# Performance work log

Hardware: AMD Instinct MI355X
Metric: run time of the kernel (lower is better)

Reference implementation:

```python
import jax, jax.numpy as jnp
import numpy as np

N = 100000
E = 1600000
NEG_SLOPE = 0.2


def _param(key, shape, scale=0.05):
    return jax.random.normal(key, shape, dtype=jnp.float32) * scale


def setup_inputs() -> dict:
    key = jax.random.key(0)
    ks = jax.random.split(key, 16)
    x = jax.random.normal(ks[0], (N, 128), dtype=jnp.float32)
    edge_index = jax.random.randint(ks[1], (2, E), 0, N, dtype=jnp.int64)
    # layer 1: 128 -> (H=2, C=64), concat
    W1 = _param(ks[2], (128, 2 * 64)); a_src1 = _param(ks[3], (2, 64)); a_dst1 = _param(ks[4], (2, 64)); b1 = jnp.zeros((128,), jnp.float32)
    # layer 2: 128 -> (H=2, C=64), concat
    W2 = _param(ks[5], (128, 2 * 64)); a_src2 = _param(ks[6], (2, 64)); a_dst2 = _param(ks[7], (2, 64)); b2 = jnp.zeros((128,), jnp.float32)
    # layer 3: 128 -> (H=1, C=64), mean (concat=False)
    W3 = _param(ks[8], (128, 1 * 64)); a_src3 = _param(ks[9], (1, 64)); a_dst3 = _param(ks[10], (1, 64)); b3 = jnp.zeros((64,), jnp.float32)
    return {"x": x, "edge_index": edge_index,
            "W1": W1, "a_src1": a_src1, "a_dst1": a_dst1, "b1": b1,
            "W2": W2, "a_src2": a_src2, "a_dst2": a_dst2, "b2": b2,
            "W3": W3, "a_src3": a_src3, "a_dst3": a_dst3, "b3": b3}


def gat_layer(x, src, dst, W, a_src, a_dst, b, concat):
    H, C = a_src.shape
    n = x.shape[0]
    h = (x @ W).reshape(n, H, C)                      # [N,H,C]
    # per-node attention logits (avoid [E,H,C] gather for the score step)
    al_s = jnp.sum(h * a_src[None], axis=-1)          # [N,H]
    al_d = jnp.sum(h * a_dst[None], axis=-1)          # [N,H]
    e = al_s[src] + al_d[dst]                         # [E',H]
    e = jnp.where(e > 0, e, NEG_SLOPE * e)            # LeakyReLU(0.2)
    # scatter-softmax over incoming edges per destination node
    m = jax.ops.segment_max(e, dst, num_segments=n)   # [N,H]
    ex = jnp.exp(e - m[dst])
    z = jax.ops.segment_sum(ex, dst, num_segments=n)  # [N,H]
    alpha = ex / z[dst]                               # [E',H]
    msg = h[src] * alpha[:, :, None]                  # [E',H,C]
    out = jax.ops.segment_sum(msg, dst, num_segments=n)  # [N,H,C]
    out = out.reshape(n, H * C) if concat else out.mean(axis=1)
    return out + b


def reference(x, edge_index, W1, a_src1, a_dst1, b1, W2, a_src2, a_dst2, b2, W3, a_src3, a_dst3, b3):
    n = x.shape[0]
    loop = jnp.arange(n, dtype=edge_index.dtype)
    src = jnp.concatenate([edge_index[0], loop])      # add self-loops (PyG default)
    dst = jnp.concatenate([edge_index[1], loop])
    h = gat_layer(x, src, dst, W1, a_src1, a_dst1, b1, True)
    h = jax.nn.relu(h)
    h = gat_layer(h, src, dst, W2, a_src2, a_dst2, b2, True)
    h = jax.nn.relu(h)
    return gat_layer(h, src, dst, W3, a_src3, a_dst3, b3, False)
```

## Files before the change

### kernel.cpp

```cpp
#include <hip/hip_runtime.h>

#define NEG_SLOPE 0.2f
#define BUK_SHIFT 9
#define BUK_SIZE 512
#define BUK_CAP 16384

typedef unsigned short u16;
typedef __attribute__((ext_vector_type(4))) float f4v;
typedef _Float16 h8 __attribute__((ext_vector_type(8)));

__device__ __forceinline__ u16 f2h_bits(_Float16 h) {
    union { _Float16 f; u16 u; } c;
    c.f = h;
    return c.u;
}


__launch_bounds__(256)
__global__ void k_binscatter(const int* __restrict__ ei, int* g_cnt, int* buckets,
                             int E, int nb) {
    __shared__ int lcnt[256], lbase[256], lcur[256];
    int t = threadIdx.x;
    if (t < nb) {
        lcnt[t] = 0;
        lcur[t] = 0;
    }
    __syncthreads();
    int tile0 = blockIdx.x * 4096;
    int pk[16], bk[16];
#pragma unroll
    for (int k = 0; k < 16; k++) {
        int idx = tile0 + k * 256 + t;
        bk[k] = -1;
        if (idx < E) {
            int s = ei[idx];
            int d = ei[E + idx];
            bk[k] = d >> BUK_SHIFT;
            pk[k] = (s << BUK_SHIFT) | (d & (BUK_SIZE - 1));
            atomicAdd(&lcnt[bk[k]], 1);
        }
    }
    __syncthreads();
    if (t < nb && lcnt[t] > 0) lbase[t] = atomicAdd(&g_cnt[t], lcnt[t]);
    __syncthreads();
#pragma unroll
    for (int k = 0; k < 16; k++) {
        if (bk[k] >= 0) {
            int p = lbase[bk[k]] + atomicAdd(&lcur[bk[k]], 1);
            if (p < BUK_CAP) buckets[(bk[k] << 14) + p] = pk[k];
        }
    }
}

__launch_bounds__(512)
__global__ void k_csr(const int* __restrict__ g_cnt, const int* __restrict__ buckets,
                      int* csr_ptr, int* csr_src, int n, int nb) {
    __shared__ int lcnt[512], lsc[512], lcur[512], bsc[512];
    int b = blockIdx.x;
    int t = threadIdx.x;
    int nodes = min(BUK_SIZE, n - b * BUK_SIZE);
    int cnt = min(g_cnt[b], BUK_CAP);
    const int* bp = &buckets[b << 14];

    int bv = 0;
    if (t < nb) bv = min(g_cnt[t], BUK_CAP) + min(BUK_SIZE, n - t * BUK_SIZE);
    bsc[t] = bv;
    __syncthreads();
    for (int off = 1; off < 512; off <<= 1) {
        int x = (t >= off) ? bsc[t - off] : 0;
        __syncthreads();
        bsc[t] += x;
        __syncthreads();
    }
    int boff = bsc[b] - (cnt + nodes);
    int total = bsc[nb - 1];
    __syncthreads();

    lcnt[t] = 0;
    __syncthreads();
    for (int i = t; i < cnt; i += 512) atomicAdd(&lcnt[bp[i] & (BUK_SIZE - 1)], 1);
    __syncthreads();
    int myc = (t < nodes) ? (lcnt[t] + 1) : 0;
    lsc[t] = myc;
    __syncthreads();
    for (int off = 1; off < 512; off <<= 1) {
        int x = (t >= off) ? lsc[t - off] : 0;
        __syncthreads();
        lsc[t] += x;
        __syncthreads();
    }
    int excl = lsc[t] - myc;
    lcur[t] = excl;
    if (t < nodes) csr_ptr[b * BUK_SIZE + t] = boff + excl;
    if (b == nb - 1 && t == 0) csr_ptr[n] = total;
    __syncthreads();
    for (int i = t; i < cnt; i += 512) {
        int v = bp[i];
        int ld = v & (BUK_SIZE - 1);
        int p = atomicAdd(&lcur[ld], 1);
        csr_src[boff + p] = v >> BUK_SHIFT;
    }
    if (t < nodes) {
        int p = atomicAdd(&lcur[t], 1);
        csr_src[boff + p] = b * BUK_SIZE + t;
    }
}


__global__ void k_wsplit_all(const float* __restrict__ W1, const float* __restrict__ W2,
                             const float* __restrict__ W3, u16* __restrict__ T1h,
                             u16* __restrict__ T1l, u16* __restrict__ T2h,
                             u16* __restrict__ T2l, u16* __restrict__ T3h,
                             u16* __restrict__ T3l, int* __restrict__ g_cnt) {
    int t = blockIdx.x * 256 + threadIdx.x;
    if (t < 256) g_cnt[t] = 0;
    const float* W;
    u16 *Th, *Tl;
    int M, idx;
    if (t < 16384) {
        W = W1; Th = T1h; Tl = T1l; M = 128; idx = t;
    } else if (t < 32768) {
        W = W2; Th = T2h; Tl = T2l; M = 128; idx = t - 16384;
    } else if (t < 40960) {
        W = W3; Th = T3h; Tl = T3l; M = 64; idx = t - 32768;
    } else {
        return;
    }
    int c = idx >> 7, k = idx & 127;
    float v = W[(size_t)k * M + c];
    _Float16 h = (_Float16)v;
    _Float16 l = (_Float16)(v - (float)h);
    int ct = c >> 4, ch = k >> 5, q = (k >> 3) & 3, j = k & 7;
    size_t addr = ((size_t)ct * 4 + ch) * 512 + ((c & 15) + 16 * q) * 8 + j;
    Th[addr] = f2h_bits(h);
    Tl[addr] = f2h_bits(l);
}


__global__ void k_wa(const float* __restrict__ W1, const float* __restrict__ as1,
                     const float* __restrict__ ad1, const float* __restrict__ W2,
                     const float* __restrict__ as2, const float* __restrict__ ad2,
                     const float* __restrict__ W3, const float* __restrict__ as3,
                     const float* __restrict__ ad3, u16* __restrict__ T1h,
                     u16* __restrict__ T1l, u16* __restrict__ T2h, u16* __restrict__ T2l,
                     u16* __restrict__ T3h, u16* __restrict__ T3l) {
    int t = blockIdx.x * 256 + threadIdx.x;
    if (t >= 6144) return;
    int layer = t >> 11;
    int rem = t & 2047;
    int k = rem >> 4;
    int c = rem & 15;
    const float *W, *as, *ad;
    u16 *Th, *Tl;
    int M, CT, nc;
    if (layer == 0) {
        W = W1; as = as1; ad = ad1; Th = T1h; Tl = T1l; M = 128; CT = 8; nc = 4;
    } else if (layer == 1) {
        W = W2; as = as2; ad = ad2; Th = T2h; Tl = T2l; M = 128; CT = 8; nc = 4;
    } else {
        W = W3; as = as3; ad = ad3; Th = T3h; Tl = T3l; M = 64; CT = 4; nc = 2;
    }
    float val = 0.f;
    if (c < nc) {
        int side, hh;
        if (nc == 4) { side = c >> 1; hh = c & 1; }
        else { side = c; hh = 0; }
        const float* a = side ? ad : as;
        for (int j = 0; j < 64; j++)
            val += W[(size_t)k * M + hh * 64 + j] * a[hh * 64 + j];
    }
    _Float16 h = (_Float16)val;
    _Float16 l = (_Float16)(val - (float)h);
    int ch = k >> 5, q = (k >> 3) & 3, j = k & 7;
    size_t addr = ((size_t)CT * 4 + ch) * 512 + ((size_t)(c + 16 * q)) * 8 + j;
    Th[addr] = f2h_bits(h);
    Tl[addr] = f2h_bits(l);
}


__device__ __forceinline__ void load_split_f32(const float* __restrict__ X, int row,
                                               int koff, int N, h8& hi, h8& lo) {
    float v[8];
    if (row < N) {
        float4 a = *(const float4*)&X[(size_t)row * 128 + koff];
        float4 b = *(const float4*)&X[(size_t)row * 128 + koff + 4];
        v[0] = a.x; v[1] = a.y; v[2] = a.z; v[3] = a.w;
        v[4] = b.x; v[5] = b.y; v[6] = b.z; v[7] = b.w;
    } else {
#pragma unroll
        for (int i = 0; i < 8; i++) v[i] = 0.f;
    }
    union { h8 s; _Float16 u[8]; } H, L;
#pragma unroll
    for (int i = 0; i < 8; i++) {
        H.u[i] = (_Float16)v[i];
        L.u[i] = (_Float16)(v[i] - (float)H.u[i]);
    }
    hi = H.s;
    lo = L.s;
}

template <int M, bool FP32X>
__launch_bounds__(256)
__global__ void k_gemm_mfma(const float* __restrict__ Xf, const u16* __restrict__ XH,
                            const u16* __restrict__ WTh, const u16* __restrict__ WTl,
                            _Float16* __restrict__ Hout, float* __restrict__ als,
                            float* __restrict__ ald, int nrows) {
    const int CT = M / 16;
    const int CTX = CT + 1;
    const int H = (M == 128) ? 2 : 1;
    int tid = threadIdx.x;
    int wv = tid >> 6, lane = tid & 63;
    int q = lane >> 4, nl = lane & 15;
    int R0 = blockIdx.x * 128 + wv * 32;
    int rt0 = R0 >> 4;

    f4v acc[2][CTX];
    f4v z4 = {0.f, 0.f, 0.f, 0.f};
#pragma unroll
    for (int rt = 0; rt < 2; rt++)
#pragma unroll
        for (int ct = 0; ct < CTX; ct++) acc[rt][ct] = z4;

#pragma unroll
    for (int ch = 0; ch < 4; ch++) {
        h8 ah0, al0, ah1, al1;
        if (FP32X) {
            int koff = ch * 32 + q * 8;
            load_split_f32(Xf, R0 + nl, koff, nrows, ah0, al0);
            load_split_f32(Xf, R0 + 16 + nl, koff, nrows, ah1, al1);
        } else {
            size_t a0 = ((size_t)rt0 * 4 + ch) * 512 + lane * 8;
            size_t a1 = ((size_t)(rt0 + 1) * 4 + ch) * 512 + lane * 8;
            ah0 = *(const h8*)&XH[a0];
            ah1 = *(const h8*)&XH[a1];
        }
#pragma unroll
        for (int ct = 0; ct < CTX; ct++) {
            size_t bb = ((size_t)ct * 4 + ch) * 512 + lane * 8;
            h8 bh = *(const h8*)&WTh[bb];
            h8 bl = *(const h8*)&WTl[bb];
            acc[0][ct] = __builtin_amdgcn_mfma_f32_16x16x32_f16(ah0, bh, acc[0][ct], 0, 0, 0);
            acc[0][ct] = __builtin_amdgcn_mfma_f32_16x16x32_f16(ah0, bl, acc[0][ct], 0, 0, 0);
            acc[1][ct] = __builtin_amdgcn_mfma_f32_16x16x32_f16(ah1, bh, acc[1][ct], 0, 0, 0);
            acc[1][ct] = __builtin_amdgcn_mfma_f32_16x16x32_f16(ah1, bl, acc[1][ct], 0, 0, 0);
            if (FP32X) {
                acc[0][ct] = __builtin_amdgcn_mfma_f32_16x16x32_f16(al0, bh, acc[0][ct], 0, 0, 0);
                acc[1][ct] = __builtin_amdgcn_mfma_f32_16x16x32_f16(al1, bh, acc[1][ct], 0, 0, 0);
            }
        }
    }

#pragma unroll
    for (int rt = 0; rt < 2; rt++)
#pragma unroll
        for (int ct = 0; ct < CT; ct++)
#pragma unroll
            for (int r = 0; r < 4; r++) {
                int row = R0 + rt * 16 + q * 4 + r;
                if (row < nrows) Hout[(size_t)row * M + ct * 16 + nl] = (_Float16)acc[rt][ct][r];
            }

    if (nl < 2 * H) {
#pragma unroll
        for (int rt = 0; rt < 2; rt++)
#pragma unroll
            for (int r = 0; r < 4; r++) {
                int row = R0 + rt * 16 + q * 4 + r;
                if (row < nrows) {
                    float v = acc[rt][CT][r];
                    if (H == 2) {
                        float* dstp = (nl < 2) ? als : ald;
                        dstp[(size_t)row * 2 + (nl & 1)] = v;
                    } else {
                        float* dstp = (nl == 0) ? als : ald;
                        dstp[row] = v;
                    }
                }
            }
    }
}


__launch_bounds__(256)
__global__ void k_agg128(const int* __restrict__ ptr, const int* __restrict__ srcv,
                         const _Float16* __restrict__ Hh, const float* __restrict__ als,
                         const float* __restrict__ ald, const float* __restrict__ bias,
                         u16* __restrict__ OutX, int n) {
    int wvg = (blockIdx.x * blockDim.x + threadIdx.x) >> 6;
    int lane = threadIdx.x & 63;
    int nn = lane >> 4;
    int gl = lane & 15;
    int wid = wvg * 4 + nn;
    bool valid = wid < n;
    int widc = valid ? wid : (n - 1);
    int start = ptr[widc];
    int deg = valid ? (ptr[widc + 1] - start) : 0;
    int md = deg;
    md = max(md, __shfl_xor(md, 16));
    md = max(md, __shfl_xor(md, 32));
    float2 adv = *(const float2*)&ald[(size_t)widc * 2];
    int hsel = gl >> 3;
    int coff = gl * 8;
    float z0 = 0.f, z1 = 0.f;
    float acc[8];
#pragma unroll
    for (int c = 0; c < 8; c++) acc[c] = 0.f;

    for (int base = 0; base < md; base += 16) {
        int i = base + gl;
        int s_l = 0;
        float ex0 = 0.f, ex1 = 0.f;
        if (i < deg) {
            s_l = srcv[start + i];
            float2 av = *(const float2*)&als[(size_t)s_l * 2];
            float e0 = av.x + adv.x;
            e0 = e0 > 0.f ? e0 : NEG_SLOPE * e0;
            ex0 = __expf(e0);
            float e1 = av.y + adv.y;
            e1 = e1 > 0.f ? e1 : NEG_SLOPE * e1;
            ex1 = __expf(e1);
        }
        z0 += ex0;
        z1 += ex1;
        int cnt = min(16, md - base);
        for (int jp = 0; jp < cnt; jp += 4) {
            int nk = min(4, cnt - jp);
            h8 hv[4];
            float w[4];
#pragma unroll
            for (int k = 0; k < 4; k++) {
                if (k < nk) {
                    int j = nn * 16 + jp + k;
                    int s = __shfl(s_l, j);
                    float w0 = __shfl(ex0, j);
                    float w1 = __shfl(ex1, j);
                    w[k] = hsel ? w1 : w0;
                    hv[k] = *(const h8*)&Hh[(size_t)s * 128 + coff];
                }
            }
#pragma unroll
            for (int k = 0; k < 4; k++) {
                if (k < nk) {
#pragma unroll
                    for (int c = 0; c < 8; c++)
                        acc[c] = fmaf(w[k], (float)hv[k][c], acc[c]);
                }
            }
        }
    }

#pragma unroll
    for (int m = 1; m <= 8; m <<= 1) {
        z0 += __shfl_xor(z0, m);
        z1 += __shfl_xor(z1, m);
    }
    if (valid) {
        float zinv = hsel ? (1.f / z1) : (1.f / z0);
        float4 b0 = *(const float4*)&bias[coff];
        float4 b1 = *(const float4*)&bias[coff + 4];
        float bb[8] = {b0.x, b0.y, b0.z, b0.w, b1.x, b1.y, b1.z, b1.w};
        union { _Float16 f[8]; h8 v; } O;
#pragma unroll
        for (int c = 0; c < 8; c++) {
            float o = fmaxf(fmaf(acc[c], zinv, bb[c]), 0.f);
            O.f[c] = (_Float16)o;
        }
        int ch = coff >> 5, qq = (coff >> 3) & 3;
        size_t tb = ((size_t)(wid >> 4) * 4 + ch) * 512 + ((size_t)((wid & 15) + 16 * qq)) * 8;
        *(h8*)&OutX[tb] = O.v;
    }
}


__launch_bounds__(256)
__global__ void k_agg64(const int* __restrict__ ptr, const int* __restrict__ srcv,
                        const _Float16* __restrict__ Hh, const float* __restrict__ als,
                        const float* __restrict__ ald, const float* __restrict__ bias,
                        float* __restrict__ Out, int n) {
    int wvg = (blockIdx.x * blockDim.x + threadIdx.x) >> 6;
    int lane = threadIdx.x & 63;
    int nn = lane >> 3;
    int gl = lane & 7;
    int wid = wvg * 8 + nn;
    bool valid = wid < n;
    int widc = valid ? wid : (n - 1);
    int start = ptr[widc];
    int deg = valid ? (ptr[widc + 1] - start) : 0;
    int md = deg;
    md = max(md, __shfl_xor(md, 8));
    md = max(md, __shfl_xor(md, 16));
    md = max(md, __shfl_xor(md, 32));
    float ad0 = ald[widc];
    int coff = gl * 8;
    float z = 0.f;
    float acc[8];
#pragma unroll
    for (int c = 0; c < 8; c++) acc[c] = 0.f;

    for (int base = 0; base < md; base += 8) {
        int i = base + gl;
        int s_l = 0;
        float ex0 = 0.f;
        if (i < deg) {
            s_l = srcv[start + i];
            float e = als[s_l] + ad0;
            e = e > 0.f ? e : NEG_SLOPE * e;
            ex0 = __expf(e);
        }
        z += ex0;
        int cnt = min(8, md - base);
        for (int jp = 0; jp < cnt; jp += 4) {
            int nk = min(4, cnt - jp);
            h8 hv[4];
            float w[4];
#pragma unroll
            for (int k = 0; k < 4; k++) {
                if (k < nk) {
                    int j = nn * 8 + jp + k;
                    int s = __shfl(s_l, j);
                    w[k] = __shfl(ex0, j);
                    hv[k] = *(const h8*)&Hh[(size_t)s * 64 + coff];
                }
            }
#pragma unroll
            for (int k = 0; k < 4; k++) {
                if (k < nk) {
#pragma unroll
                    for (int c = 0; c < 8; c++)
                        acc[c] = fmaf(w[k], (float)hv[k][c], acc[c]);
                }
            }
        }
    }

#pragma unroll
    for (int m = 1; m <= 4; m <<= 1) z += __shfl_xor(z, m);
    if (valid) {
        float zinv = 1.f / z;
        float4 b0 = *(const float4*)&bias[coff];
        float4 b1 = *(const float4*)&bias[coff + 4];
        float4 o1, o2;
        o1.x = fmaf(acc[0], zinv, b0.x);
        o1.y = fmaf(acc[1], zinv, b0.y);
        o1.z = fmaf(acc[2], zinv, b0.z);
        o1.w = fmaf(acc[3], zinv, b0.w);
        o2.x = fmaf(acc[4], zinv, b1.x);
        o2.y = fmaf(acc[5], zinv, b1.y);
        o2.z = fmaf(acc[6], zinv, b1.z);
        o2.w = fmaf(acc[7], zinv, b1.w);
        *(float4*)&Out[(size_t)wid * 64 + coff] = o1;
        *(float4*)&Out[(size_t)wid * 64 + coff + 4] = o2;
    }
}


extern "C" void kernel_launch(void* const* d_in, const int* in_sizes, int n_in,
                              void* d_out, int out_size, void* d_ws, size_t ws_size,
                              hipStream_t stream) {
    const float* x = (const float*)d_in[0];
    const int* ei = (const int*)d_in[1];
    const float* W1 = (const float*)d_in[2];
    const float* as1 = (const float*)d_in[3];
    const float* ad1 = (const float*)d_in[4];
    const float* b1 = (const float*)d_in[5];
    const float* W2 = (const float*)d_in[6];
    const float* as2 = (const float*)d_in[7];
    const float* ad2 = (const float*)d_in[8];
    const float* b2 = (const float*)d_in[9];
    const float* W3 = (const float*)d_in[10];
    const float* as3 = (const float*)d_in[11];
    const float* ad3 = (const float*)d_in[12];
    const float* b3 = (const float*)d_in[13];

    const int N = in_sizes[0] / 128;
    const int E = in_sizes[1] / 2;
    const int NB = (N + BUK_SIZE - 1) / BUK_SIZE;
    const int Npad = (N + 127) & ~127;

    char* p = (char*)d_ws;
    auto alloc = [&](size_t bytes) -> char* {
        char* r = p;
        p += (bytes + 255) & ~(size_t)255;
        return r;
    };
    int* g_cnt = (int*)alloc(256 * 4);
    int* buckets = (int*)alloc((size_t)NB * BUK_CAP * 4);
    int* csr_ptr = (int*)alloc((size_t)(N + 1) * 4);
    int* csr_src = (int*)alloc((size_t)(E + N) * 4);
    float* als = (float*)alloc((size_t)N * 2 * 4);
    float* aldv = (float*)alloc((size_t)N * 2 * 4);
    _Float16* Hbuf = (_Float16*)alloc((size_t)N * 128 * 2);
    u16* XH = (u16*)alloc((size_t)Npad * 128 * 2);
    u16* WT1h = (u16*)alloc(9 * 2048 * 2);
    u16* WT1l = (u16*)alloc(9 * 2048 * 2);
    u16* WT2h = (u16*)alloc(9 * 2048 * 2);
    u16* WT2l = (u16*)alloc(9 * 2048 * 2);
    u16* WT3h = (u16*)alloc(5 * 2048 * 2);
    u16* WT3l = (u16*)alloc(5 * 2048 * 2);

    const int nbG = Npad / 128;
    const int waves128 = (N + 3) / 4;
    const int nbAgg128 = (waves128 + 3) / 4;
    const int waves64 = (N + 7) / 8;
    const int nbAgg64 = (waves64 + 3) / 4;
    const int nbTile = (E + 4095) / 4096;

    k_wsplit_all<<<160, 256, 0, stream>>>(W1, W2, W3, WT1h, WT1l, WT2h, WT2l, WT3h,
                                          WT3l, g_cnt);
    k_wa<<<24, 256, 0, stream>>>(W1, as1, ad1, W2, as2, ad2, W3, as3, ad3,
                                 WT1h, WT1l, WT2h, WT2l, WT3h, WT3l);

    k_binscatter<<<nbTile, 256, 0, stream>>>(ei, g_cnt, buckets, E, NB);
    k_csr<<<NB, 512, 0, stream>>>(g_cnt, buckets, csr_ptr, csr_src, N, NB);

    k_gemm_mfma<128, true><<<nbG, 256, 0, stream>>>(x, nullptr, WT1h, WT1l,
                                                    Hbuf, als, aldv, N);
    k_agg128<<<nbAgg128, 256, 0, stream>>>(csr_ptr, csr_src, Hbuf, als, aldv, b1, XH, N);

    k_gemm_mfma<128, false><<<nbG, 256, 0, stream>>>(nullptr, XH, WT2h, WT2l,
                                                     Hbuf, als, aldv, N);
    k_agg128<<<nbAgg128, 256, 0, stream>>>(csr_ptr, csr_src, Hbuf, als, aldv, b2, XH, N);

    k_gemm_mfma<64, false><<<nbG, 256, 0, stream>>>(nullptr, XH, WT3h, WT3l,
                                                    Hbuf, als, aldv, N);
    k_agg64<<<nbAgg64, 256, 0, stream>>>(csr_ptr, csr_src, Hbuf, als, aldv, b3,
                                         (float*)d_out, N);
}
```

Measured before the change: 418.6 us.

## Merge preprocessing kernels and overlap CSR build with first-layer GEMM

Result: faster. 400.5 us, median of 2 (-4.3%).

```diff
diff --git a/kernel.cpp b/kernel.cpp
--- a/kernel.cpp
+++ b/kernel.cpp
@@ -13,168 +13,6 @@
     union { _Float16 f; u16 u; } c;
     c.f = h;
     return c.u;
-}
-
-
-__launch_bounds__(256)
-__global__ void k_binscatter(const int* __restrict__ ei, int* g_cnt, int* buckets,
-                             int E, int nb) {
-    __shared__ int lcnt[256], lbase[256], lcur[256];
-    int t = threadIdx.x;
-    if (t < nb) {
-        lcnt[t] = 0;
-        lcur[t] = 0;
-    }
-    __syncthreads();
-    int tile0 = blockIdx.x * 4096;
-    int pk[16], bk[16];
-#pragma unroll
-    for (int k = 0; k < 16; k++) {
-        int idx = tile0 + k * 256 + t;
-        bk[k] = -1;
-        if (idx < E) {
-            int s = ei[idx];
-            int d = ei[E + idx];
-            bk[k] = d >> BUK_SHIFT;
-            pk[k] = (s << BUK_SHIFT) | (d & (BUK_SIZE - 1));
-            atomicAdd(&lcnt[bk[k]], 1);
-        }
-    }
-    __syncthreads();
-    if (t < nb && lcnt[t] > 0) lbase[t] = atomicAdd(&g_cnt[t], lcnt[t]);
-    __syncthreads();
-#pragma unroll
-    for (int k = 0; k < 16; k++) {
-        if (bk[k] >= 0) {
-            int p = lbase[bk[k]] + atomicAdd(&lcur[bk[k]], 1);
-            if (p < BUK_CAP) buckets[(bk[k] << 14) + p] = pk[k];
-        }
-    }
-}
-
-__launch_bounds__(512)
-__global__ void k_csr(const int* __restrict__ g_cnt, const int* __restrict__ buckets,
-                      int* csr_ptr, int* csr_src, int n, int nb) {
-    __shared__ int lcnt[512], lsc[512], lcur[512], bsc[512];
-    int b = blockIdx.x;
-    int t = threadIdx.x;
-    int nodes = min(BUK_SIZE, n - b * BUK_SIZE);
-    int cnt = min(g_cnt[b], BUK_CAP);
-    const int* bp = &buckets[b << 14];
-
-    int bv = 0;
-    if (t < nb) bv = min(g_cnt[t], BUK_CAP) + min(BUK_SIZE, n - t * BUK_SIZE);
-    bsc[t] = bv;
-    __syncthreads();
-    for (int off = 1; off < 512; off <<= 1) {
-        int x = (t >= off) ? bsc[t - off] : 0;
-        __syncthreads();
-        bsc[t] += x;
-        __syncthreads();
-    }
-    int boff = bsc[b] - (cnt + nodes);
-    int total = bsc[nb - 1];
-    __syncthreads();
-
-    lcnt[t] = 0;
-    __syncthreads();
-    for (int i = t; i < cnt; i += 512) atomicAdd(&lcnt[bp[i] & (BUK_SIZE - 1)], 1);
-    __syncthreads();
-    int myc = (t < nodes) ? (lcnt[t] + 1) : 0;
-    lsc[t] = myc;
-    __syncthreads();
-    for (int off = 1; off < 512; off <<= 1) {
-        int x = (t >= off) ? lsc[t - off] : 0;
-        __syncthreads();
-        lsc[t] += x;
-        __syncthreads();
-    }
-    int excl = lsc[t] - myc;
-    lcur[t] = excl;
-    if (t < nodes) csr_ptr[b * BUK_SIZE + t] = boff + excl;
-    if (b == nb - 1 && t == 0) csr_ptr[n] = total;
-    __syncthreads();
-    for (int i = t; i < cnt; i += 512) {
-        int v = bp[i];
-        int ld = v & (BUK_SIZE - 1);
-        int p = atomicAdd(&lcur[ld], 1);
-        csr_src[boff + p] = v >> BUK_SHIFT;
-    }
-    if (t < nodes) {
-        int p = atomicAdd(&lcur[t], 1);
-        csr_src[boff + p] = b * BUK_SIZE + t;
-    }
-}
-
-
-__global__ void k_wsplit_all(const float* __restrict__ W1, const float* __restrict__ W2,
-                             const float* __restrict__ W3, u16* __restrict__ T1h,
-                             u16* __restrict__ T1l, u16* __restrict__ T2h,
-                             u16* __restrict__ T2l, u16* __restrict__ T3h,
-                             u16* __restrict__ T3l, int* __restrict__ g_cnt) {
-    int t = blockIdx.x * 256 + threadIdx.x;
-    if (t < 256) g_cnt[t] = 0;
-    const float* W;
-    u16 *Th, *Tl;
-    int M, idx;
-    if (t < 16384) {
-        W = W1; Th = T1h; Tl = T1l; M = 128; idx = t;
-    } else if (t < 32768) {
-        W = W2; Th = T2h; Tl = T2l; M = 128; idx = t - 16384;
-    } else if (t < 40960) {
-        W = W3; Th = T3h; Tl = T3l; M = 64; idx = t - 32768;
-    } else {
-        return;
-    }
-    int c = idx >> 7, k = idx & 127;
-    float v = W[(size_t)k * M + c];
-    _Float16 h = (_Float16)v;
-    _Float16 l = (_Float16)(v - (float)h);
-    int ct = c >> 4, ch = k >> 5, q = (k >> 3) & 3, j = k & 7;
-    size_t addr = ((size_t)ct * 4 + ch) * 512 + ((c & 15) + 16 * q) * 8 + j;
-    Th[addr] = f2h_bits(h);
-    Tl[addr] = f2h_bits(l);
-}
-
-
-__global__ void k_wa(const float* __restrict__ W1, const float* __restrict__ as1,
-                     const float* __restrict__ ad1, const float* __restrict__ W2,
-                     const float* __restrict__ as2, const float* __restrict__ ad2,
-                     const float* __restrict__ W3, const float* __restrict__ as3,
-                     const float* __restrict__ ad3, u16* __restrict__ T1h,
-                     u16* __restrict__ T1l, u16* __restrict__ T2h, u16* __restrict__ T2l,
-                     u16* __restrict__ T3h, u16* __restrict__ T3l) {
-    int t = blockIdx.x * 256 + threadIdx.x;
-    if (t >= 6144) return;
-    int layer = t >> 11;
-    int rem = t & 2047;
-    int k = rem >> 4;
-    int c = rem & 15;
-    const float *W, *as, *ad;
-    u16 *Th, *Tl;
-    int M, CT, nc;
-    if (layer == 0) {
-        W = W1; as = as1; ad = ad1; Th = T1h; Tl = T1l; M = 128; CT = 8; nc = 4;
-    } else if (layer == 1) {
-        W = W2; as = as2; ad = ad2; Th = T2h; Tl = T2l; M = 128; CT = 8; nc = 4;
-    } else {
-        W = W3; as = as3; ad = ad3; Th = T3h; Tl = T3l; M = 64; CT = 4; nc = 2;
-    }
-    float val = 0.f;
-    if (c < nc) {
-        int side, hh;
-        if (nc == 4) { side = c >> 1; hh = c & 1; }
-        else { side = c; hh = 0; }
-        const float* a = side ? ad : as;
-        for (int j = 0; j < 64; j++)
-            val += W[(size_t)k * M + hh * 64 + j] * a[hh * 64 + j];
-    }
-    _Float16 h = (_Float16)val;
-    _Float16 l = (_Float16)(val - (float)h);
-    int ch = k >> 5, q = (k >> 3) & 3, j = k & 7;
-    size_t addr = ((size_t)CT * 4 + ch) * 512 + ((size_t)(c + 16 * q)) * 8 + j;
-    Th[addr] = f2h_bits(h);
-    Tl[addr] = f2h_bits(l);
 }
 
 
@@ -201,18 +39,20 @@
 }
 
 template <int M, bool FP32X>
-__launch_bounds__(256)
-__global__ void k_gemm_mfma(const float* __restrict__ Xf, const u16* __restrict__ XH,
-                            const u16* __restrict__ WTh, const u16* __restrict__ WTl,
-                            _Float16* __restrict__ Hout, float* __restrict__ als,
-                            float* __restrict__ ald, int nrows) {
+__device__ __forceinline__ void gemm_body(int gb, const float* __restrict__ Xf,
+                                          const u16* __restrict__ XH,
+                                          const u16* __restrict__ WTh,
+                                          const u16* __restrict__ WTl,
+                                          _Float16* __restrict__ Hout,
+                                          float* __restrict__ als,
+                                          float* __restrict__ ald, int nrows) {
     const int CT = M / 16;
     const int CTX = CT + 1;
     const int H = (M == 128) ? 2 : 1;
     int tid = threadIdx.x;
     int wv = tid >> 6, lane = tid & 63;
     int q = lane >> 4, nl = lane & 15;
-    int R0 = blockIdx.x * 128 + wv * 32;
+    int R0 = gb * 256 + wv * 32;
     int rt0 = R0 >> 4;
 
     f4v acc[2][CTX];
@@ -278,6 +118,178 @@
                     }
                 }
             }
+    }
+}
+
+template <int M, bool FP32X>
+__launch_bounds__(512)
+__global__ void k_gemm(const float* __restrict__ Xf, const u16* __restrict__ XH,
+                       const u16* __restrict__ WTh, const u16* __restrict__ WTl,
+                       _Float16* __restrict__ Hout, float* __restrict__ als,
+                       float* __restrict__ ald, int nrows) {
+    gemm_body<M, FP32X>(blockIdx.x, Xf, XH, WTh, WTl, Hout, als, ald, nrows);
+}
+
+
+__launch_bounds__(512)
+__global__ void k_d1(const int* __restrict__ ei, int* g_cnt, int* buckets, int E, int nb,
+                     int nbin, const float* __restrict__ W1, const float* __restrict__ as1,
+                     const float* __restrict__ ad1, const float* __restrict__ W2,
+                     const float* __restrict__ as2, const float* __restrict__ ad2,
+                     const float* __restrict__ W3, const float* __restrict__ as3,
+                     const float* __restrict__ ad3, u16* __restrict__ T1h,
+                     u16* __restrict__ T1l, u16* __restrict__ T2h, u16* __restrict__ T2l,
+                     u16* __restrict__ T3h, u16* __restrict__ T3l) {
+    __shared__ int lcnt[256], lbase[256], lcur[256];
+    int b = blockIdx.x;
+    int t = threadIdx.x;
+    if (b < nbin) {
+        if (t < nb) {
+            lcnt[t] = 0;
+            lcur[t] = 0;
+        }
+        __syncthreads();
+        int tile0 = b * 4096;
+        int pk[8], bk[8];
+#pragma unroll
+        for (int k = 0; k < 8; k++) {
+            int idx = tile0 + k * 512 + t;
+            bk[k] = -1;
+            if (idx < E) {
+                int s = ei[idx];
+                int d = ei[E + idx];
+                bk[k] = d >> BUK_SHIFT;
+                pk[k] = (s << BUK_SHIFT) | (d & (BUK_SIZE - 1));
+                atomicAdd(&lcnt[bk[k]], 1);
+            }
+        }
+        __syncthreads();
+        if (t < nb && lcnt[t] > 0) lbase[t] = atomicAdd(&g_cnt[t], lcnt[t]);
+        __syncthreads();
+#pragma unroll
+        for (int k = 0; k < 8; k++) {
+            if (bk[k] >= 0) {
+                int p = lbase[bk[k]] + atomicAdd(&lcur[bk[k]], 1);
+                if (p < BUK_CAP) buckets[(bk[k] << 14) + p] = pk[k];
+            }
+        }
+        return;
+    }
+    int rb = b - nbin;
+    if (rb < 80) {
+        int idx = rb * 512 + t;
+        const float* W;
+        u16 *Th, *Tl;
+        int M, li;
+        if (idx < 16384) {
+            W = W1; Th = T1h; Tl = T1l; M = 128; li = idx;
+        } else if (idx < 32768) {
+            W = W2; Th = T2h; Tl = T2l; M = 128; li = idx - 16384;
+        } else {
+            W = W3; Th = T3h; Tl = T3l; M = 64; li = idx - 32768;
+        }
+        int c = li >> 7, k = li & 127;
+        float v = W[(size_t)k * M + c];
+        _Float16 h = (_Float16)v;
+        _Float16 l = (_Float16)(v - (float)h);
+        int ct = c >> 4, ch = k >> 5, q = (k >> 3) & 3, j = k & 7;
+        size_t addr = ((size_t)ct * 4 + ch) * 512 + ((c & 15) + 16 * q) * 8 + j;
+        Th[addr] = f2h_bits(h);
+        Tl[addr] = f2h_bits(l);
+    } else {
+        int idx = (rb - 80) * 512 + t;
+        if (idx >= 6144) return;
+        int layer = idx >> 11;
+        int rem = idx & 2047;
+        int k = rem >> 4;
+        int c = rem & 15;
+        const float *W, *as, *ad;
+        u16 *Th, *Tl;
+        int M, CT, nc;
+        if (layer == 0) {
+            W = W1; as = as1; ad = ad1; Th = T1h; Tl = T1l; M = 128; CT = 8; nc = 4;
+        } else if (layer == 1) {
+            W = W2; as = as2; ad = ad2; Th = T2h; Tl = T2l; M = 128; CT = 8; nc = 4;
+        } else {
+            W = W3; as = as3; ad = ad3; Th = T3h; Tl = T3l; M = 64; CT = 4; nc = 2;
+        }
+        float val = 0.f;
+        if (c < nc) {
+            int side, hh;
+            if (nc == 4) { side = c >> 1; hh = c & 1; }
+            else { side = c; hh = 0; }
+            const float* a = side ? ad : as;
+            for (int j = 0; j < 64; j++)
+                val += W[(size_t)k * M + hh * 64 + j] * a[hh * 64 + j];
+        }
+        _Float16 h = (_Float16)val;
+        _Float16 l = (_Float16)(val - (float)h);
+        int ch = k >> 5, q = (k >> 3) & 3, j = k & 7;
+        size_t addr = ((size_t)CT * 4 + ch) * 512 + ((size_t)(c + 16 * q)) * 8 + j;
+        Th[addr] = f2h_bits(h);
+        Tl[addr] = f2h_bits(l);
+    }
+}
+
+
+__launch_bounds__(512)
+__global__ void k_d2(const int* __restrict__ g_cnt, const int* __restrict__ buckets,
+                     int* csr_ptr, int* csr_src, int n, int nb,
+                     const float* __restrict__ x, const u16* __restrict__ WTh,
+                     const u16* __restrict__ WTl, _Float16* __restrict__ Hout,
+                     float* __restrict__ als, float* __restrict__ ald) {
+    __shared__ int lcnt[512], lsc[512], lcur[512], bsc[512];
+    int b = blockIdx.x;
+    int t = threadIdx.x;
+    if (b >= nb) {
+        gemm_body<128, true>(b - nb, x, nullptr, WTh, WTl, Hout, als, ald, n);
+        return;
+    }
+    int nodes = min(BUK_SIZE, n - b * BUK_SIZE);
+    int cnt = min(g_cnt[b], BUK_CAP);
+    const int* bp = &buckets[b << 14];
+
+    int bv = 0;
+    if (t < nb) bv = min(g_cnt[t], BUK_CAP) + min(BUK_SIZE, n - t * BUK_SIZE);
+    bsc[t] = bv;
+    __syncthreads();
+    for (int off = 1; off < 512; off <<= 1) {
+        int xx = (t >= off) ? bsc[t - off] : 0;
+        __syncthreads();
+        bsc[t] += xx;
+        __syncthreads();
+    }
+    int boff = bsc[b] - (cnt + nodes);
+    int total = bsc[nb - 1];
+    __syncthreads();
+
+    lcnt[t] = 0;
+    __syncthreads();
+    for (int i = t; i < cnt; i += 512) atomicAdd(&lcnt[bp[i] & (BUK_SIZE - 1)], 1);
+    __syncthreads();
+    int myc = (t < nodes) ? (lcnt[t] + 1) : 0;
+    lsc[t] = myc;
+    __syncthreads();
+    for (int off = 1; off < 512; off <<= 1) {
+        int xx = (t >= off) ? lsc[t - off] : 0;
+        __syncthreads();
+        lsc[t] += xx;
+        __syncthreads();
+    }
+    int excl = lsc[t] - myc;
+    lcur[t] = excl;
+    if (t < nodes) csr_ptr[b * BUK_SIZE + t] = boff + excl;
+    if (b == nb - 1 && t == 0) csr_ptr[n] = total;
+    __syncthreads();
+    for (int i = t; i < cnt; i += 512) {
+        int v = bp[i];
+        int ld = v & (BUK_SIZE - 1);
+        int p = atomicAdd(&lcur[ld], 1);
+        csr_src[boff + p] = v >> BUK_SHIFT;
+    }
+    if (t < nodes) {
+        int p = atomicAdd(&lcur[t], 1);
+        csr_src[boff + p] = b * BUK_SIZE + t;
     }
 }
 
@@ -476,7 +488,7 @@
     const int N = in_sizes[0] / 128;
     const int E = in_sizes[1] / 2;
     const int NB = (N + BUK_SIZE - 1) / BUK_SIZE;
-    const int Npad = (N + 127) & ~127;
+    const int Npad = (N + 255) & ~255;
 
     char* p = (char*)d_ws;
     auto alloc = [&](size_t bytes) -> char* {
@@ -499,31 +511,30 @@
     u16* WT3h = (u16*)alloc(5 * 2048 * 2);
     u16* WT3l = (u16*)alloc(5 * 2048 * 2);
 
-    const int nbG = Npad / 128;
+    const int GTOT = Npad / 256;
+    const int NBIN = (E + 4095) / 4096;
     const int waves128 = (N + 3) / 4;
     const int nbAgg128 = (waves128 + 3) / 4;
     const int waves64 = (N + 7) / 8;
     const int nbAgg64 = (waves64 + 3) / 4;
-    const int nbTile = (E + 4095) / 4096;
-
-    k_wsplit_all<<<160, 256, 0, stream>>>(W1, W2, W3, WT1h, WT1l, WT2h, WT2l, WT3h,
-                                          WT3l, g_cnt);
-    k_wa<<<24, 256, 0, stream>>>(W1, as1, ad1, W2, as2, ad2, W3, as3, ad3,
-                                 WT1h, WT1l, WT2h, WT2l, WT3h, WT3l);
-
-    k_binscatter<<<nbTile, 256, 0, stream>>>(ei, g_cnt, buckets, E, NB);
-    k_csr<<<NB, 512, 0, stream>>>(g_cnt, buckets, csr_ptr, csr_src, N, NB);
-
-    k_gemm_mfma<128, true><<<nbG, 256, 0, stream>>>(x, nullptr, WT1h, WT1l,
-                                                    Hbuf, als, aldv, N);
+
+    hipMemsetAsync(g_cnt, 0, 256 * 4, stream);
+
+    k_d1<<<NBIN + 92, 512, 0, stream>>>(ei, g_cnt, buckets, E, NB, NBIN,
+                                        W1, as1, ad1, W2, as2, ad2, W3, as3, ad3,
+                                        WT1h, WT1l, WT2h, WT2l, WT3h, WT3l);
+
+    k_d2<<<NB + GTOT, 512, 0, stream>>>(g_cnt, buckets, csr_ptr, csr_src, N, NB,
+                                        x, WT1h, WT1l, Hbuf, als, aldv);
+
     k_agg128<<<nbAgg128, 256, 0, stream>>>(csr_ptr, csr_src, Hbuf, als, aldv, b1, XH, N);
 
-    k_gemm_mfma<128, false><<<nbG, 256, 0, stream>>>(nullptr, XH, WT2h, WT2l,
-                                                     Hbuf, als, aldv, N);
+    k_gemm<128, false><<<GTOT, 512, 0, stream>>>(nullptr, XH, WT2h, WT2l,
+                                                 Hbuf, als, aldv, N);
     k_agg128<<<nbAgg128, 256, 0, stream>>>(csr_ptr, csr_src, Hbuf, als, aldv, b2, XH, N);
 
-    k_gemm_mfma<64, false><<<nbG, 256, 0, stream>>>(nullptr, XH, WT3h, WT3l,
-                                                    Hbuf, als, aldv, N);
+    k_gemm<64, false><<<GTOT, 512, 0, stream>>>(nullptr, XH, WT3h, WT3l,
+                                                Hbuf, als, aldv, N);
     k_agg64<<<nbAgg64, 256, 0, stream>>>(csr_ptr, csr_src, Hbuf, als, aldv, b3,
                                          (float*)d_out, N);
 }
```
